# Kernel tuning notes

Hardware: AMD Instinct MI355X
Metric: run time of the kernel (lower is better)

Reference implementation:

```python
import jax, jax.numpy as jnp
import numpy as np

DIM = 256
HEADS = 8
DIM_HEAD = 64
INNER = HEADS * DIM_HEAD  # 512
WIN = 7
N = WIN * WIN  # 49
B = 4096
EPS = 1e-5


def _rel_pos_indices(w):
    pos = np.arange(w)
    gi, gj = np.meshgrid(pos, pos, indexing='ij')
    grid = np.stack([gi.reshape(-1), gj.reshape(-1)], axis=-1)  # (w*w, 2)
    rel = grid[:, None, :] - grid[None, :, :] + (w - 1)          # (n, n, 2)
    return (rel[..., 0] * (2 * w - 1) + rel[..., 1]).astype(np.int32)  # (n, n)


def setup_inputs() -> dict:
    key = jax.random.key(0)
    ks = jax.random.split(key, 6)
    x = jax.random.normal(ks[0], (B, N, DIM), dtype=jnp.float32)
    gamma = jnp.ones((DIM,), dtype=jnp.float32)
    beta = jnp.zeros((DIM,), dtype=jnp.float32)
    W_qkv = jax.random.normal(ks[1], (DIM, 3 * INNER), dtype=jnp.float32) * (DIM ** -0.5)
    W_out = jax.random.normal(ks[2], (INNER, DIM), dtype=jnp.float32) * (INNER ** -0.5)
    b_out = jnp.zeros((DIM,), dtype=jnp.float32)
    bias_table = jax.random.normal(ks[3], ((2 * WIN - 1) ** 2, HEADS), dtype=jnp.float32) * 0.02
    rel_idx = jnp.asarray(_rel_pos_indices(WIN))  # (49, 49) int32
    return {"x": x, "gamma": gamma, "beta": beta, "W_qkv": W_qkv,
            "W_out": W_out, "b_out": b_out, "bias_table": bias_table,
            "rel_idx": rel_idx}


def reference(x, gamma, beta, W_qkv, W_out, b_out, bias_table, rel_idx):
    # LayerNorm
    mu = jnp.mean(x, axis=-1, keepdims=True)
    var = jnp.mean((x - mu) ** 2, axis=-1, keepdims=True)
    xn = (x - mu) * jax.lax.rsqrt(var + EPS) * gamma + beta
    # QKV projection (no bias)
    qkv = xn @ W_qkv                                   # (b, n, 3*inner)
    q, k, v = jnp.split(qkv, 3, axis=-1)
    def to_heads(t):
        b, n, _ = t.shape
        return t.reshape(b, n, HEADS, DIM_HEAD).transpose(0, 2, 1, 3)  # b h n d
    q, k, v = to_heads(q), to_heads(k), to_heads(v)
    q = q * (DIM_HEAD ** -0.5)
    sim = jnp.einsum('bhid,bhjd->bhij', q, k)          # (b, h, n, n)
    bias = bias_table[rel_idx]                         # (n, n, h)
    sim = sim + bias.transpose(2, 0, 1)[None]          # add (h, n, n)
    attn = jax.nn.softmax(sim, axis=-1)
    out = jnp.einsum('bhij,bhjd->bhid', attn, v)       # (b, h, n, d)
    out = out.transpose(0, 2, 1, 3).reshape(x.shape[0], N, INNER)
    return out @ W_out + b_out
```

## Files before the change

kernel.cpp:

```cpp
#include <hip/hip_runtime.h>
#include <hip/hip_bf16.h>
#include <stdint.h>

#define NTOK 49

typedef __bf16 bf16x8 __attribute__((ext_vector_type(8)));
typedef float f32x4 __attribute__((ext_vector_type(4)));

__device__ __forceinline__ uint16_t f2bf(float f){
  uint32_t x = __float_as_uint(f);
  uint32_t r = (x + 0x7fffu + ((x >> 16) & 1u)) >> 16;
  return (uint16_t)r;
}

#define LDS_LD8(buf, row, kelem) \
  __builtin_bit_cast(bf16x8, *(const uint4*)((const char*)(buf) + (row)*128 + ((((kelem)*2)) ^ ((((row))&7)<<4))))

__global__ void prep_kernel(const float* __restrict__ Wqkv,
                            const float* __restrict__ Wout,
                            const float* __restrict__ btab,
                            const int* __restrict__ ridx,
                            uint16_t* __restrict__ WqkvT,
                            uint16_t* __restrict__ WoutT,
                            float* __restrict__ biasPre){
  const int T1 = 1536*256, T2 = 256*512, T3 = 8*2401;
  for (int i = blockIdx.x*blockDim.x + threadIdx.x; i < T1+T2+T3; i += gridDim.x*blockDim.x){
    if (i < T1){ int n = i/256, k = i%256; WqkvT[i] = f2bf(Wqkv[k*1536 + n]); }
    else if (i < T1+T2){ int j = i - T1; int n = j/512, k = j%512; WoutT[j] = f2bf(Wout[k*256 + n]); }
    else { int j = i - T1 - T2; int h = j/2401, ij = j%2401; biasPre[j] = btab[ridx[ij]*8 + h]; }
  }
}

__global__ __launch_bounds__(256, 2)
void maxvit_fused(const float* __restrict__ x,
                  const float* __restrict__ gamma,
                  const float* __restrict__ beta,
                  const uint16_t* __restrict__ WqkvT,
                  const uint16_t* __restrict__ WoutT,
                  const float*    __restrict__ bout,
                  const float*    __restrict__ biasPre,
                  float* __restrict__ out)
{
  __shared__ uint16_t xn[50*256];
  __shared__ uint16_t qs[50*64];
  __shared__ uint16_t ks[50*64];
  __shared__ uint16_t ps[50*64];
  __shared__ uint16_t vt[64*64];

  const int b    = blockIdx.x;
  const int tid  = threadIdx.x;
  const int wave = tid >> 6;
  const int lane = tid & 63;
  const int lo   = lane & 15;
  const int g    = lane >> 4;
  const f32x4 fzero = {0.f, 0.f, 0.f, 0.f};

  {
    const int c0 = lane * 4;
    float4 gm = *(const float4*)(gamma + c0);
    float4 bt = *(const float4*)(beta  + c0);
    for (int r = wave; r < 50; r += 4){
      char* dst = (char*)xn + r*512 + ((c0*2) ^ ((r&7)<<4));
      if (r < NTOK){
        float4 u = *(const float4*)(x + ((size_t)(b*NTOK + r))*256 + c0);
        float s  = u.x+u.y+u.z+u.w;
        float ss = u.x*u.x+u.y*u.y+u.z*u.z+u.w*u.w;
        #pragma unroll
        for (int d = 1; d < 64; d <<= 1){ s += __shfl_xor(s, d); ss += __shfl_xor(ss, d); }
        float mu  = s  * (1.0f/256.0f);
        float var = ss * (1.0f/256.0f) - mu*mu;
        float rs  = rsqrtf(var + 1e-5f);
        ushort4 o;
        o.x = f2bf((u.x-mu)*rs*gm.x+bt.x);
        o.y = f2bf((u.y-mu)*rs*gm.y+bt.y);
        o.z = f2bf((u.z-mu)*rs*gm.z+bt.z);
        o.w = f2bf((u.w-mu)*rs*gm.w+bt.w);
        *(ushort4*)dst = o;
      } else {
        ushort4 z; z.x = z.y = z.z = z.w = 0;
        *(ushort4*)dst = z;
      }
    }
  }
  __syncthreads();

  f32x4 outacc[4][4];
  #pragma unroll
  for (int m = 0; m < 4; m++)
    #pragma unroll
    for (int n = 0; n < 4; n++) outacc[m][n] = fzero;

  for (int h = 0; h < 8; ++h){
    f32x4 aq[4], ak[4], av[4];
    #pragma unroll
    for (int m = 0; m < 4; m++){ aq[m] = fzero; ak[m] = fzero; av[m] = fzero; }
    const uint16_t* pq = WqkvT + (size_t)(       h*64 + wave*16 + lo)*256;
    const uint16_t* pk = WqkvT + (size_t)( 512 + h*64 + wave*16 + lo)*256;
    const uint16_t* pv = WqkvT + (size_t)(1024 + h*64 + wave*16 + lo)*256;
    #pragma unroll
    for (int k0 = 0; k0 < 256; k0 += 32){
      const int kb = k0 + g*8;
      bf16x8 afr[4];
      #pragma unroll
      for (int m = 0; m < 4; m++){
        int row = m*16 + lo;
        if (m == 3) row = (row < 49) ? row : 49;
        afr[m] = __builtin_bit_cast(bf16x8,
          *(const uint4*)((const char*)xn + row*512 + ((kb*2) ^ ((row&7)<<4))));
      }
      bf16x8 fq = __builtin_bit_cast(bf16x8, *(const uint4*)(pq + kb));
      bf16x8 fk = __builtin_bit_cast(bf16x8, *(const uint4*)(pk + kb));
      bf16x8 fv = __builtin_bit_cast(bf16x8, *(const uint4*)(pv + kb));
      #pragma unroll
      for (int m = 0; m < 4; m++){
        aq[m] = __builtin_amdgcn_mfma_f32_16x16x32_bf16(afr[m], fq, aq[m], 0, 0, 0);
        ak[m] = __builtin_amdgcn_mfma_f32_16x16x32_bf16(afr[m], fk, ak[m], 0, 0, 0);
        av[m] = __builtin_amdgcn_mfma_f32_16x16x32_bf16(afr[m], fv, av[m], 0, 0, 0);
      }
    }
    {
      const int d = wave*16 + lo;
      #pragma unroll
      for (int m = 0; m < 4; m++){
        #pragma unroll
        for (int r = 0; r < 4; r++){
          const int token = m*16 + g*4 + r;
          const int tok   = (token < 49) ? token : 49;
          *(uint16_t*)((char*)qs + tok*128 + ((d*2) ^ ((tok&7)<<4))) = f2bf(aq[m][r]*0.125f);
          *(uint16_t*)((char*)ks + tok*128 + ((d*2) ^ ((tok&7)<<4))) = f2bf(ak[m][r]);
          *(uint16_t*)((char*)vt + d*128 + ((token*2) ^ ((d&7)<<4))) = f2bf(av[m][r]);
        }
      }
    }
    __syncthreads();

    f32x4 s[4];
    #pragma unroll
    for (int n = 0; n < 4; n++) s[n] = fzero;
    {
      int qrow = wave*16 + lo; qrow = (qrow < 49) ? qrow : 49;
      bf16x8 a0 = LDS_LD8(qs, qrow, g*8);
      bf16x8 a1 = LDS_LD8(qs, qrow, 32 + g*8);
      #pragma unroll
      for (int n = 0; n < 4; n++){
        int krow = n*16 + lo;
        if (n == 3) krow = (krow < 49) ? krow : 49;
        bf16x8 b0 = LDS_LD8(ks, krow, g*8);
        bf16x8 b1 = LDS_LD8(ks, krow, 32 + g*8);
        s[n] = __builtin_amdgcn_mfma_f32_16x16x32_bf16(a0, b0, s[n], 0, 0, 0);
        s[n] = __builtin_amdgcn_mfma_f32_16x16x32_bf16(a1, b1, s[n], 0, 0, 0);
      }
    }
    {
      const float* bp = biasPre + h*2401;
      #pragma unroll
      for (int n = 0; n < 4; n++){
        const int j = n*16 + lo;
        #pragma unroll
        for (int r = 0; r < 4; r++){
          const int i = wave*16 + g*4 + r;
          float v = s[n][r];
          if (j < NTOK){ if (i < NTOK) v += bp[i*49 + j]; }
          else v = -1e30f;
          s[n][r] = v;
        }
      }
      float mx[4], sm[4];
      #pragma unroll
      for (int r = 0; r < 4; r++){
        float m0 = fmaxf(fmaxf(s[0][r], s[1][r]), fmaxf(s[2][r], s[3][r]));
        #pragma unroll
        for (int d = 1; d < 16; d <<= 1) m0 = fmaxf(m0, __shfl_xor(m0, d));
        mx[r] = m0;
        sm[r] = 0.f;
      }
      #pragma unroll
      for (int n = 0; n < 4; n++)
        #pragma unroll
        for (int r = 0; r < 4; r++){ float p = __expf(s[n][r] - mx[r]); s[n][r] = p; sm[r] += p; }
      #pragma unroll
      for (int r = 0; r < 4; r++){
        float t = sm[r];
        #pragma unroll
        for (int d = 1; d < 16; d <<= 1) t += __shfl_xor(t, d);
        sm[r] = 1.0f / t;
      }
      #pragma unroll
      for (int n = 0; n < 4; n++){
        const int j = n*16 + lo;
        #pragma unroll
        for (int r = 0; r < 4; r++){
          int i = wave*16 + g*4 + r; i = (i < 49) ? i : 49;
          *(uint16_t*)((char*)ps + i*128 + ((j*2) ^ ((i&7)<<4))) = f2bf(s[n][r]*sm[r]);
        }
      }
    }

    f32x4 o[4];
    #pragma unroll
    for (int n = 0; n < 4; n++) o[n] = fzero;
    {
      int prow = wave*16 + lo; prow = (prow < 49) ? prow : 49;
      bf16x8 a0 = LDS_LD8(ps, prow, g*8);
      bf16x8 a1 = LDS_LD8(ps, prow, 32 + g*8);
      #pragma unroll
      for (int n = 0; n < 4; n++){
        const int vrow = n*16 + lo;
        bf16x8 b0 = LDS_LD8(vt, vrow, g*8);
        bf16x8 b1 = LDS_LD8(vt, vrow, 32 + g*8);
        o[n] = __builtin_amdgcn_mfma_f32_16x16x32_bf16(a0, b0, o[n], 0, 0, 0);
        o[n] = __builtin_amdgcn_mfma_f32_16x16x32_bf16(a1, b1, o[n], 0, 0, 0);
      }
    }
    #pragma unroll
    for (int n = 0; n < 4; n++){
      const int d = n*16 + lo;
      #pragma unroll
      for (int r = 0; r < 4; r++){
        int token = wave*16 + g*4 + r; token = (token < 49) ? token : 49;
        *(uint16_t*)((char*)ps + token*128 + ((d*2) ^ ((token&7)<<4))) = f2bf(o[n][r]);
      }
    }
    __syncthreads();

    #pragma unroll
    for (int kk = 0; kk < 2; ++kk){
      const int kb = kk*32 + g*8;
      bf16x8 afr[4];
      #pragma unroll
      for (int m = 0; m < 4; m++){
        int row = m*16 + lo;
        if (m == 3) row = (row < 49) ? row : 49;
        afr[m] = LDS_LD8(ps, row, kb);
      }
      #pragma unroll
      for (int n = 0; n < 4; n++){
        const int ncol = wave*64 + n*16 + lo;
        bf16x8 bb = __builtin_bit_cast(bf16x8,
          *(const uint4*)(WoutT + (size_t)ncol*512 + h*64 + kb));
        #pragma unroll
        for (int m = 0; m < 4; m++)
          outacc[m][n] = __builtin_amdgcn_mfma_f32_16x16x32_bf16(afr[m], bb, outacc[m][n], 0, 0, 0);
      }
    }
  }

  #pragma unroll
  for (int n = 0; n < 4; n++){
    const int col = wave*64 + n*16 + lo;
    const float bo = bout[col];
    #pragma unroll
    for (int m = 0; m < 4; m++){
      #pragma unroll
      for (int r = 0; r < 4; r++){
        const int token = m*16 + g*4 + r;
        if (token < NTOK)
          out[((size_t)(b*NTOK + token))*256 + col] = outacc[m][n][r] + bo;
      }
    }
  }
}

extern "C" void kernel_launch(void* const* d_in, const int* in_sizes, int n_in,
                              void* d_out, int out_size, void* d_ws, size_t ws_size,
                              hipStream_t stream){
  const float* x     = (const float*)d_in[0];
  const float* gamma = (const float*)d_in[1];
  const float* beta  = (const float*)d_in[2];
  const float* Wqkv  = (const float*)d_in[3];
  const float* Wout  = (const float*)d_in[4];
  const float* bout  = (const float*)d_in[5];
  const float* btab  = (const float*)d_in[6];
  const int*   ridx  = (const int*)d_in[7];

  uint16_t* WqkvT   = (uint16_t*)d_ws;
  uint16_t* WoutT   = (uint16_t*)((char*)d_ws + 786432);
  float*    biasPre = (float*)((char*)d_ws + 786432 + 262144);

  prep_kernel<<<512, 256, 0, stream>>>(Wqkv, Wout, btab, ridx, WqkvT, WoutT, biasPre);
  maxvit_fused<<<4096, 256, 0, stream>>>(x, gamma, beta, WqkvT, WoutT, bout, biasPre,
                                         (float*)d_out);
}
```

Measured before the change: 1.083 ms.

## Double-buffer per-head Q/K/V and overlap next-head projection with attention

```diff
diff --git a/kernel.cpp b/kernel.cpp
--- a/kernel.cpp
+++ b/kernel.cpp
@@ -42,10 +42,11 @@
                   float* __restrict__ out)
 {
   __shared__ uint16_t xn[50*256];
-  __shared__ uint16_t qs[50*64];
-  __shared__ uint16_t ks[50*64];
+  __shared__ uint16_t qs[2][50*64];
+  __shared__ uint16_t ks[2][50*64];
+  __shared__ uint16_t vt[2][64*64];
   __shared__ uint16_t ps[50*64];
-  __shared__ uint16_t vt[64*64];
+  __shared__ uint16_t os[50*64];
 
   const int b    = blockIdx.x;
   const int tid  = threadIdx.x;
@@ -90,13 +91,12 @@
     #pragma unroll
     for (int n = 0; n < 4; n++) outacc[m][n] = fzero;
 
-  for (int h = 0; h < 8; ++h){
-    f32x4 aq[4], ak[4], av[4];
-    #pragma unroll
-    for (int m = 0; m < 4; m++){ aq[m] = fzero; ak[m] = fzero; av[m] = fzero; }
-    const uint16_t* pq = WqkvT + (size_t)(       h*64 + wave*16 + lo)*256;
-    const uint16_t* pk = WqkvT + (size_t)( 512 + h*64 + wave*16 + lo)*256;
-    const uint16_t* pv = WqkvT + (size_t)(1024 + h*64 + wave*16 + lo)*256;
+  auto projQK = [&](int hh, int bi){
+    f32x4 aq[4], ak[4];
+    #pragma unroll
+    for (int m = 0; m < 4; m++){ aq[m] = fzero; ak[m] = fzero; }
+    const uint16_t* pq = WqkvT + (size_t)(       hh*64 + wave*16 + lo)*256;
+    const uint16_t* pk = WqkvT + (size_t)( 512 + hh*64 + wave*16 + lo)*256;
     #pragma unroll
     for (int k0 = 0; k0 < 256; k0 += 32){
       const int kb = k0 + g*8;
@@ -110,43 +110,85 @@
       }
       bf16x8 fq = __builtin_bit_cast(bf16x8, *(const uint4*)(pq + kb));
       bf16x8 fk = __builtin_bit_cast(bf16x8, *(const uint4*)(pk + kb));
-      bf16x8 fv = __builtin_bit_cast(bf16x8, *(const uint4*)(pv + kb));
       #pragma unroll
       for (int m = 0; m < 4; m++){
         aq[m] = __builtin_amdgcn_mfma_f32_16x16x32_bf16(afr[m], fq, aq[m], 0, 0, 0);
         ak[m] = __builtin_amdgcn_mfma_f32_16x16x32_bf16(afr[m], fk, ak[m], 0, 0, 0);
+      }
+    }
+    uint16_t* qb = qs[bi];
+    uint16_t* kb2 = ks[bi];
+    const int d = wave*16 + lo;
+    #pragma unroll
+    for (int m = 0; m < 4; m++){
+      #pragma unroll
+      for (int r = 0; r < 4; r++){
+        const int token = m*16 + g*4 + r;
+        const int tok   = (token < 49) ? token : 49;
+        *(uint16_t*)((char*)qb  + tok*128 + ((d*2) ^ ((tok&7)<<4))) = f2bf(aq[m][r]*0.125f);
+        *(uint16_t*)((char*)kb2 + tok*128 + ((d*2) ^ ((tok&7)<<4))) = f2bf(ak[m][r]);
+      }
+    }
+  };
+
+  auto projV = [&](int hh, int bi){
+    f32x4 av[4];
+    #pragma unroll
+    for (int m = 0; m < 4; m++) av[m] = fzero;
+    const uint16_t* pv = WqkvT + (size_t)(1024 + hh*64 + wave*16 + lo)*256;
+    #pragma unroll
+    for (int k0 = 0; k0 < 256; k0 += 32){
+      const int kb = k0 + g*8;
+      bf16x8 afr[4];
+      #pragma unroll
+      for (int m = 0; m < 4; m++){
+        int row = m*16 + lo;
+        if (m == 3) row = (row < 49) ? row : 49;
+        afr[m] = __builtin_bit_cast(bf16x8,
+          *(const uint4*)((const char*)xn + row*512 + ((kb*2) ^ ((row&7)<<4))));
+      }
+      bf16x8 fv = __builtin_bit_cast(bf16x8, *(const uint4*)(pv + kb));
+      #pragma unroll
+      for (int m = 0; m < 4; m++)
         av[m] = __builtin_amdgcn_mfma_f32_16x16x32_bf16(afr[m], fv, av[m], 0, 0, 0);
-      }
-    }
-    {
-      const int d = wave*16 + lo;
-      #pragma unroll
-      for (int m = 0; m < 4; m++){
-        #pragma unroll
-        for (int r = 0; r < 4; r++){
-          const int token = m*16 + g*4 + r;
-          const int tok   = (token < 49) ? token : 49;
-          *(uint16_t*)((char*)qs + tok*128 + ((d*2) ^ ((tok&7)<<4))) = f2bf(aq[m][r]*0.125f);
-          *(uint16_t*)((char*)ks + tok*128 + ((d*2) ^ ((tok&7)<<4))) = f2bf(ak[m][r]);
-          *(uint16_t*)((char*)vt + d*128 + ((token*2) ^ ((d&7)<<4))) = f2bf(av[m][r]);
-        }
-      }
-    }
-    __syncthreads();
+    }
+    uint16_t* vb = vt[bi];
+    const int d = wave*16 + lo;
+    #pragma unroll
+    for (int m = 0; m < 4; m++){
+      #pragma unroll
+      for (int r = 0; r < 4; r++){
+        const int token = m*16 + g*4 + r;
+        *(uint16_t*)((char*)vb + d*128 + ((token*2) ^ ((d&7)<<4))) = f2bf(av[m][r]);
+      }
+    }
+  };
+
+  projQK(0, 0);
+  projV(0, 0);
+  __syncthreads();
+
+  for (int h = 0; h < 8; ++h){
+    const int cur = h & 1, nxt = cur ^ 1;
+    const uint16_t* qsc = qs[cur];
+    const uint16_t* ksc = ks[cur];
+    const uint16_t* vtc = vt[cur];
+
+    if (h < 7) projQK(h+1, nxt);
 
     f32x4 s[4];
     #pragma unroll
     for (int n = 0; n < 4; n++) s[n] = fzero;
     {
       int qrow = wave*16 + lo; qrow = (qrow < 49) ? qrow : 49;
-      bf16x8 a0 = LDS_LD8(qs, qrow, g*8);
-      bf16x8 a1 = LDS_LD8(qs, qrow, 32 + g*8);
+      bf16x8 a0 = LDS_LD8(qsc, qrow, g*8);
+      bf16x8 a1 = LDS_LD8(qsc, qrow, 32 + g*8);
       #pragma unroll
       for (int n = 0; n < 4; n++){
         int krow = n*16 + lo;
         if (n == 3) krow = (krow < 49) ? krow : 49;
-        bf16x8 b0 = LDS_LD8(ks, krow, g*8);
-        bf16x8 b1 = LDS_LD8(ks, krow, 32 + g*8);
+        bf16x8 b0 = LDS_LD8(ksc, krow, g*8);
+        bf16x8 b1 = LDS_LD8(ksc, krow, 32 + g*8);
         s[n] = __builtin_amdgcn_mfma_f32_16x16x32_bf16(a0, b0, s[n], 0, 0, 0);
         s[n] = __builtin_amdgcn_mfma_f32_16x16x32_bf16(a1, b1, s[n], 0, 0, 0);
       }
@@ -206,8 +248,8 @@
       #pragma unroll
       for (int n = 0; n < 4; n++){
         const int vrow = n*16 + lo;
-        bf16x8 b0 = LDS_LD8(vt, vrow, g*8);
-        bf16x8 b1 = LDS_LD8(vt, vrow, 32 + g*8);
+        bf16x8 b0 = LDS_LD8(vtc, vrow, g*8);
+        bf16x8 b1 = LDS_LD8(vtc, vrow, 32 + g*8);
         o[n] = __builtin_amdgcn_mfma_f32_16x16x32_bf16(a0, b0, o[n], 0, 0, 0);
         o[n] = __builtin_amdgcn_mfma_f32_16x16x32_bf16(a1, b1, o[n], 0, 0, 0);
       }
@@ -218,10 +260,12 @@
       #pragma unroll
       for (int r = 0; r < 4; r++){
         int token = wave*16 + g*4 + r; token = (token < 49) ? token : 49;
-        *(uint16_t*)((char*)ps + token*128 + ((d*2) ^ ((token&7)<<4))) = f2bf(o[n][r]);
+        *(uint16_t*)((char*)os + token*128 + ((d*2) ^ ((token&7)<<4))) = f2bf(o[n][r]);
       }
     }
     __syncthreads();
+
+    if (h < 7) projV(h+1, nxt);
 
     #pragma unroll
     for (int kk = 0; kk < 2; ++kk){
@@ -231,7 +275,7 @@
       for (int m = 0; m < 4; m++){
         int row = m*16 + lo;
         if (m == 3) row = (row < 49) ? row : 49;
-        afr[m] = LDS_LD8(ps, row, kb);
+        afr[m] = LDS_LD8(os, row, kb);
       }
       #pragma unroll
       for (int n = 0; n < 4; n++){
@@ -243,6 +287,7 @@
           outacc[m][n] = __builtin_amdgcn_mfma_f32_16x16x32_bf16(afr[m], bb, outacc[m][n], 0, 0, 0);
       }
     }
+    __syncthreads();
   }
 
   #pragma unroll
```

Measured after the change: 870.5 us. 19.6% less time.

## Split fused MaxViT attention across eight waves per block

Applied to the files above, without the earlier changes.

```diff
diff --git a/kernel.cpp b/kernel.cpp
--- a/kernel.cpp
+++ b/kernel.cpp
@@ -31,7 +31,7 @@
   }
 }
 
-__global__ __launch_bounds__(256, 2)
+__global__ __launch_bounds__(512, 4)
 void maxvit_fused(const float* __restrict__ x,
                   const float* __restrict__ gamma,
                   const float* __restrict__ beta,
@@ -44,8 +44,9 @@
   __shared__ uint16_t xn[50*256];
   __shared__ uint16_t qs[50*64];
   __shared__ uint16_t ks[50*64];
+  __shared__ uint16_t vt[64*64];
   __shared__ uint16_t ps[50*64];
-  __shared__ uint16_t vt[64*64];
+  __shared__ uint16_t os[50*64];
 
   const int b    = blockIdx.x;
   const int tid  = threadIdx.x;
@@ -53,13 +54,15 @@
   const int lane = tid & 63;
   const int lo   = lane & 15;
   const int g    = lane >> 4;
+  const int wm   = wave & 3;
+  const int wn   = wave >> 2;
   const f32x4 fzero = {0.f, 0.f, 0.f, 0.f};
 
   {
     const int c0 = lane * 4;
     float4 gm = *(const float4*)(gamma + c0);
     float4 bt = *(const float4*)(beta  + c0);
-    for (int r = wave; r < 50; r += 4){
+    for (int r = wave; r < 50; r += 8){
       char* dst = (char*)xn + r*512 + ((c0*2) ^ ((r&7)<<4));
       if (r < NTOK){
         float4 u = *(const float4*)(x + ((size_t)(b*NTOK + r))*256 + c0);
@@ -84,61 +87,65 @@
   }
   __syncthreads();
 
-  f32x4 outacc[4][4];
+  f32x4 outacc[4][2];
   #pragma unroll
-  for (int m = 0; m < 4; m++)
-    #pragma unroll
-    for (int n = 0; n < 4; n++) outacc[m][n] = fzero;
+  for (int m = 0; m < 4; m++){ outacc[m][0] = fzero; outacc[m][1] = fzero; }
+
+  const int mt     = wave >> 1;
+  const int ntbase = (wave & 1) * 6;
 
   for (int h = 0; h < 8; ++h){
-    f32x4 aq[4], ak[4], av[4];
-    #pragma unroll
-    for (int m = 0; m < 4; m++){ aq[m] = fzero; ak[m] = fzero; av[m] = fzero; }
-    const uint16_t* pq = WqkvT + (size_t)(       h*64 + wave*16 + lo)*256;
-    const uint16_t* pk = WqkvT + (size_t)( 512 + h*64 + wave*16 + lo)*256;
-    const uint16_t* pv = WqkvT + (size_t)(1024 + h*64 + wave*16 + lo)*256;
-    #pragma unroll
-    for (int k0 = 0; k0 < 256; k0 += 32){
-      const int kb = k0 + g*8;
-      bf16x8 afr[4];
-      #pragma unroll
-      for (int m = 0; m < 4; m++){
-        int row = m*16 + lo;
-        if (m == 3) row = (row < 49) ? row : 49;
-        afr[m] = __builtin_bit_cast(bf16x8,
-          *(const uint4*)((const char*)xn + row*512 + ((kb*2) ^ ((row&7)<<4))));
-      }
-      bf16x8 fq = __builtin_bit_cast(bf16x8, *(const uint4*)(pq + kb));
-      bf16x8 fk = __builtin_bit_cast(bf16x8, *(const uint4*)(pk + kb));
-      bf16x8 fv = __builtin_bit_cast(bf16x8, *(const uint4*)(pv + kb));
-      #pragma unroll
-      for (int m = 0; m < 4; m++){
-        aq[m] = __builtin_amdgcn_mfma_f32_16x16x32_bf16(afr[m], fq, aq[m], 0, 0, 0);
-        ak[m] = __builtin_amdgcn_mfma_f32_16x16x32_bf16(afr[m], fk, ak[m], 0, 0, 0);
-        av[m] = __builtin_amdgcn_mfma_f32_16x16x32_bf16(afr[m], fv, av[m], 0, 0, 0);
-      }
-    }
     {
-      const int d = wave*16 + lo;
-      #pragma unroll
-      for (int m = 0; m < 4; m++){
+      f32x4 acc[6];
+      #pragma unroll
+      for (int t = 0; t < 6; t++) acc[t] = fzero;
+      const uint16_t* wp[6];
+      #pragma unroll
+      for (int t = 0; t < 6; t++){
+        const int nt  = ntbase + t;
+        const int sel = nt >> 2;
+        const int dt  = nt & 3;
+        wp[t] = WqkvT + (size_t)(sel*512 + h*64 + dt*16 + lo)*256;
+      }
+      int xrow = mt*16 + lo;
+      if (mt == 3) xrow = (xrow < 49) ? xrow : 49;
+      #pragma unroll
+      for (int k0 = 0; k0 < 256; k0 += 32){
+        const int kb = k0 + g*8;
+        bf16x8 afr = __builtin_bit_cast(bf16x8,
+          *(const uint4*)((const char*)xn + xrow*512 + ((kb*2) ^ ((xrow&7)<<4))));
+        #pragma unroll
+        for (int t = 0; t < 6; t++){
+          bf16x8 bb = __builtin_bit_cast(bf16x8, *(const uint4*)(wp[t] + kb));
+          acc[t] = __builtin_amdgcn_mfma_f32_16x16x32_bf16(afr, bb, acc[t], 0, 0, 0);
+        }
+      }
+      #pragma unroll
+      for (int t = 0; t < 6; t++){
+        const int nt  = ntbase + t;
+        const int sel = nt >> 2;
+        const int d   = (nt & 3)*16 + lo;
         #pragma unroll
         for (int r = 0; r < 4; r++){
-          const int token = m*16 + g*4 + r;
-          const int tok   = (token < 49) ? token : 49;
-          *(uint16_t*)((char*)qs + tok*128 + ((d*2) ^ ((tok&7)<<4))) = f2bf(aq[m][r]*0.125f);
-          *(uint16_t*)((char*)ks + tok*128 + ((d*2) ^ ((tok&7)<<4))) = f2bf(ak[m][r]);
-          *(uint16_t*)((char*)vt + d*128 + ((token*2) ^ ((d&7)<<4))) = f2bf(av[m][r]);
+          const int token = mt*16 + g*4 + r;
+          if (sel == 2){
+            *(uint16_t*)((char*)vt + d*128 + ((token*2) ^ ((d&7)<<4))) = f2bf(acc[t][r]);
+          } else {
+            const int tok = (token < 49) ? token : 49;
+            uint16_t* buf = (sel == 0) ? qs : ks;
+            const float v = (sel == 0) ? acc[t][r]*0.125f : acc[t][r];
+            *(uint16_t*)((char*)buf + tok*128 + ((d*2) ^ ((tok&7)<<4))) = f2bf(v);
+          }
         }
       }
     }
     __syncthreads();
 
-    f32x4 s[4];
-    #pragma unroll
-    for (int n = 0; n < 4; n++) s[n] = fzero;
     {
-      int qrow = wave*16 + lo; qrow = (qrow < 49) ? qrow : 49;
+      f32x4 s[4];
+      #pragma unroll
+      for (int n = 0; n < 4; n++) s[n] = fzero;
+      int qrow = wm*16 + lo; qrow = (qrow < 49) ? qrow : 49;
       bf16x8 a0 = LDS_LD8(qs, qrow, g*8);
       bf16x8 a1 = LDS_LD8(qs, qrow, 32 + g*8);
       #pragma unroll
@@ -150,15 +157,13 @@
         s[n] = __builtin_amdgcn_mfma_f32_16x16x32_bf16(a0, b0, s[n], 0, 0, 0);
         s[n] = __builtin_amdgcn_mfma_f32_16x16x32_bf16(a1, b1, s[n], 0, 0, 0);
       }
-    }
-    {
       const float* bp = biasPre + h*2401;
       #pragma unroll
       for (int n = 0; n < 4; n++){
         const int j = n*16 + lo;
         #pragma unroll
         for (int r = 0; r < 4; r++){
-          const int i = wave*16 + g*4 + r;
+          const int i = wm*16 + g*4 + r;
           float v = s[n][r];
           if (j < NTOK){ if (i < NTOK) v += bp[i*49 + j]; }
           else v = -1e30f;
@@ -185,40 +190,42 @@
         for (int d = 1; d < 16; d <<= 1) t += __shfl_xor(t, d);
         sm[r] = 1.0f / t;
       }
-      #pragma unroll
-      for (int n = 0; n < 4; n++){
-        const int j = n*16 + lo;
-        #pragma unroll
-        for (int r = 0; r < 4; r++){
-          int i = wave*16 + g*4 + r; i = (i < 49) ? i : 49;
-          *(uint16_t*)((char*)ps + i*128 + ((j*2) ^ ((i&7)<<4))) = f2bf(s[n][r]*sm[r]);
-        }
-      }
-    }
-
-    f32x4 o[4];
-    #pragma unroll
-    for (int n = 0; n < 4; n++) o[n] = fzero;
+      if (wn == 0){
+        #pragma unroll
+        for (int n = 0; n < 4; n++){
+          const int j = n*16 + lo;
+          #pragma unroll
+          for (int r = 0; r < 4; r++){
+            int i = wm*16 + g*4 + r; i = (i < 49) ? i : 49;
+            *(uint16_t*)((char*)ps + i*128 + ((j*2) ^ ((i&7)<<4))) = f2bf(s[n][r]*sm[r]);
+          }
+        }
+      }
+    }
+    __syncthreads();
+
     {
-      int prow = wave*16 + lo; prow = (prow < 49) ? prow : 49;
+      f32x4 o[2];
+      o[0] = fzero; o[1] = fzero;
+      int prow = wm*16 + lo; prow = (prow < 49) ? prow : 49;
       bf16x8 a0 = LDS_LD8(ps, prow, g*8);
       bf16x8 a1 = LDS_LD8(ps, prow, 32 + g*8);
       #pragma unroll
-      for (int n = 0; n < 4; n++){
-        const int vrow = n*16 + lo;
+      for (int n2 = 0; n2 < 2; n2++){
+        const int vrow = wn*32 + n2*16 + lo;
         bf16x8 b0 = LDS_LD8(vt, vrow, g*8);
         bf16x8 b1 = LDS_LD8(vt, vrow, 32 + g*8);
-        o[n] = __builtin_amdgcn_mfma_f32_16x16x32_bf16(a0, b0, o[n], 0, 0, 0);
-        o[n] = __builtin_amdgcn_mfma_f32_16x16x32_bf16(a1, b1, o[n], 0, 0, 0);
-      }
-    }
-    #pragma unroll
-    for (int n = 0; n < 4; n++){
-      const int d = n*16 + lo;
-      #pragma unroll
-      for (int r = 0; r < 4; r++){
-        int token = wave*16 + g*4 + r; token = (token < 49) ? token : 49;
-        *(uint16_t*)((char*)ps + token*128 + ((d*2) ^ ((token&7)<<4))) = f2bf(o[n][r]);
+        o[n2] = __builtin_amdgcn_mfma_f32_16x16x32_bf16(a0, b0, o[n2], 0, 0, 0);
+        o[n2] = __builtin_amdgcn_mfma_f32_16x16x32_bf16(a1, b1, o[n2], 0, 0, 0);
+      }
+      #pragma unroll
+      for (int n2 = 0; n2 < 2; n2++){
+        const int d = wn*32 + n2*16 + lo;
+        #pragma unroll
+        for (int r = 0; r < 4; r++){
+          int token = wm*16 + g*4 + r; token = (token < 49) ? token : 49;
+          *(uint16_t*)((char*)os + token*128 + ((d*2) ^ ((token&7)<<4))) = f2bf(o[n2][r]);
+        }
       }
     }
     __syncthreads();
@@ -231,31 +238,33 @@
       for (int m = 0; m < 4; m++){
         int row = m*16 + lo;
         if (m == 3) row = (row < 49) ? row : 49;
-        afr[m] = LDS_LD8(ps, row, kb);
-      }
-      #pragma unroll
-      for (int n = 0; n < 4; n++){
-        const int ncol = wave*64 + n*16 + lo;
+        afr[m] = LDS_LD8(os, row, kb);
+      }
+      #pragma unroll
+      for (int n2 = 0; n2 < 2; n2++){
+        const int ncol = wave*32 + n2*16 + lo;
         bf16x8 bb = __builtin_bit_cast(bf16x8,
           *(const uint4*)(WoutT + (size_t)ncol*512 + h*64 + kb));
         #pragma unroll
         for (int m = 0; m < 4; m++)
-          outacc[m][n] = __builtin_amdgcn_mfma_f32_16x16x32_bf16(afr[m], bb, outacc[m][n], 0, 0, 0);
-      }
-    }
-  }
-
-  #pragma unroll
-  for (int n = 0; n < 4; n++){
-    const int col = wave*64 + n*16 + lo;
-    const float bo = bout[col];
+          outacc[m][n2] = __builtin_amdgcn_mfma_f32_16x16x32_bf16(afr[m], bb, outacc[m][n2], 0, 0, 0);
+      }
+    }
+  }
+
+  {
+    float bo0 = bout[wave*32 + lo];
+    float bo1 = bout[wave*32 + 16 + lo];
     #pragma unroll
     for (int m = 0; m < 4; m++){
       #pragma unroll
       for (int r = 0; r < 4; r++){
         const int token = m*16 + g*4 + r;
-        if (token < NTOK)
-          out[((size_t)(b*NTOK + token))*256 + col] = outacc[m][n][r] + bo;
+        if (token < NTOK){
+          float* po = out + ((size_t)(b*NTOK + token))*256 + wave*32 + lo;
+          po[0]  = outacc[m][0][r] + bo0;
+          po[16] = outacc[m][1][r] + bo1;
+        }
       }
     }
   }
@@ -278,6 +287,6 @@
   float*    biasPre = (float*)((char*)d_ws + 786432 + 262144);
 
   prep_kernel<<<512, 256, 0, stream>>>(Wqkv, Wout, btab, ridx, WqkvT, WoutT, biasPre);
-  maxvit_fused<<<4096, 256, 0, stream>>>(x, gamma, beta, WqkvT, WoutT, bout, biasPre,
+  maxvit_fused<<<4096, 512, 0, stream>>>(x, gamma, beta, WqkvT, WoutT, bout, biasPre,
                                          (float*)d_out);
 }
```

Result: slower. 2.783 ms (+156.9%).

## Split fused attention kernel into QKV-attention and separate output-projection kernels

Applied to the files above, without the earlier changes.

```diff
diff --git a/kernel.cpp b/kernel.cpp
--- a/kernel.cpp
+++ b/kernel.cpp
@@ -15,6 +15,10 @@
 
 #define LDS_LD8(buf, row, kelem) \
   __builtin_bit_cast(bf16x8, *(const uint4*)((const char*)(buf) + (row)*128 + ((((kelem)*2)) ^ ((((row))&7)<<4))))
+#define LDS_LD8X(buf, row, kelem) \
+  __builtin_bit_cast(bf16x8, *(const uint4*)((const char*)(buf) + (row)*512 + ((((kelem)*2)) ^ ((((row))&7)<<4))))
+#define LDS_LD8O(buf, row, kelem) \
+  __builtin_bit_cast(bf16x8, *(const uint4*)((const char*)(buf) + (row)*1024 + ((((kelem)*2)) ^ ((((row))&7)<<4))))
 
 __global__ void prep_kernel(const float* __restrict__ Wqkv,
                             const float* __restrict__ Wout,
@@ -31,15 +35,13 @@
   }
 }
 
-__global__ __launch_bounds__(256, 2)
-void maxvit_fused(const float* __restrict__ x,
-                  const float* __restrict__ gamma,
-                  const float* __restrict__ beta,
-                  const uint16_t* __restrict__ WqkvT,
-                  const uint16_t* __restrict__ WoutT,
-                  const float*    __restrict__ bout,
-                  const float*    __restrict__ biasPre,
-                  float* __restrict__ out)
+__global__ __launch_bounds__(256, 3)
+void qkv_attn(const float* __restrict__ x,
+              const float* __restrict__ gamma,
+              const float* __restrict__ beta,
+              const uint16_t* __restrict__ WqkvT,
+              const float*    __restrict__ biasPre,
+              uint16_t* __restrict__ Ostg)
 {
   __shared__ uint16_t xn[50*256];
   __shared__ uint16_t qs[50*64];
@@ -84,41 +86,34 @@
   }
   __syncthreads();
 
-  f32x4 outacc[4][4];
-  #pragma unroll
-  for (int m = 0; m < 4; m++)
-    #pragma unroll
-    for (int n = 0; n < 4; n++) outacc[m][n] = fzero;
-
   for (int h = 0; h < 8; ++h){
-    f32x4 aq[4], ak[4], av[4];
-    #pragma unroll
-    for (int m = 0; m < 4; m++){ aq[m] = fzero; ak[m] = fzero; av[m] = fzero; }
-    const uint16_t* pq = WqkvT + (size_t)(       h*64 + wave*16 + lo)*256;
-    const uint16_t* pk = WqkvT + (size_t)( 512 + h*64 + wave*16 + lo)*256;
-    const uint16_t* pv = WqkvT + (size_t)(1024 + h*64 + wave*16 + lo)*256;
-    #pragma unroll
-    for (int k0 = 0; k0 < 256; k0 += 32){
-      const int kb = k0 + g*8;
-      bf16x8 afr[4];
-      #pragma unroll
-      for (int m = 0; m < 4; m++){
-        int row = m*16 + lo;
-        if (m == 3) row = (row < 49) ? row : 49;
-        afr[m] = __builtin_bit_cast(bf16x8,
-          *(const uint4*)((const char*)xn + row*512 + ((kb*2) ^ ((row&7)<<4))));
-      }
-      bf16x8 fq = __builtin_bit_cast(bf16x8, *(const uint4*)(pq + kb));
-      bf16x8 fk = __builtin_bit_cast(bf16x8, *(const uint4*)(pk + kb));
-      bf16x8 fv = __builtin_bit_cast(bf16x8, *(const uint4*)(pv + kb));
-      #pragma unroll
-      for (int m = 0; m < 4; m++){
-        aq[m] = __builtin_amdgcn_mfma_f32_16x16x32_bf16(afr[m], fq, aq[m], 0, 0, 0);
-        ak[m] = __builtin_amdgcn_mfma_f32_16x16x32_bf16(afr[m], fk, ak[m], 0, 0, 0);
-        av[m] = __builtin_amdgcn_mfma_f32_16x16x32_bf16(afr[m], fv, av[m], 0, 0, 0);
-      }
-    }
-    {
+    {
+      f32x4 aq[4], ak[4], av[4];
+      #pragma unroll
+      for (int m = 0; m < 4; m++){ aq[m] = fzero; ak[m] = fzero; av[m] = fzero; }
+      const uint16_t* pq = WqkvT + (size_t)(       h*64 + wave*16 + lo)*256;
+      const uint16_t* pk = WqkvT + (size_t)( 512 + h*64 + wave*16 + lo)*256;
+      const uint16_t* pv = WqkvT + (size_t)(1024 + h*64 + wave*16 + lo)*256;
+      #pragma unroll
+      for (int k0 = 0; k0 < 256; k0 += 32){
+        const int kb = k0 + g*8;
+        bf16x8 afr[4];
+        #pragma unroll
+        for (int m = 0; m < 4; m++){
+          int row = m*16 + lo;
+          if (m == 3) row = (row < 49) ? row : 49;
+          afr[m] = LDS_LD8X(xn, row, kb);
+        }
+        bf16x8 fq = __builtin_bit_cast(bf16x8, *(const uint4*)(pq + kb));
+        bf16x8 fk = __builtin_bit_cast(bf16x8, *(const uint4*)(pk + kb));
+        bf16x8 fv = __builtin_bit_cast(bf16x8, *(const uint4*)(pv + kb));
+        #pragma unroll
+        for (int m = 0; m < 4; m++){
+          aq[m] = __builtin_amdgcn_mfma_f32_16x16x32_bf16(afr[m], fq, aq[m], 0, 0, 0);
+          ak[m] = __builtin_amdgcn_mfma_f32_16x16x32_bf16(afr[m], fk, ak[m], 0, 0, 0);
+          av[m] = __builtin_amdgcn_mfma_f32_16x16x32_bf16(afr[m], fv, av[m], 0, 0, 0);
+        }
+      }
       const int d = wave*16 + lo;
       #pragma unroll
       for (int m = 0; m < 4; m++){
@@ -212,36 +207,76 @@
         o[n] = __builtin_amdgcn_mfma_f32_16x16x32_bf16(a1, b1, o[n], 0, 0, 0);
       }
     }
+    {
+      uint16_t* owin = Ostg + (size_t)b*(NTOK*512);
+      #pragma unroll
+      for (int n = 0; n < 4; n++){
+        const int d = n*16 + lo;
+        #pragma unroll
+        for (int r = 0; r < 4; r++){
+          const int token = wave*16 + g*4 + r;
+          if (token < NTOK)
+            owin[token*512 + h*64 + d] = f2bf(o[n][r]);
+        }
+      }
+    }
+    __syncthreads();
+  }
+}
+
+__global__ __launch_bounds__(256, 2)
+void outproj(const uint16_t* __restrict__ Ostg,
+             const uint16_t* __restrict__ WoutT,
+             const float*    __restrict__ bout,
+             float* __restrict__ out)
+{
+  __shared__ uint16_t os[50*512];
+
+  const int b    = blockIdx.x;
+  const int tid  = threadIdx.x;
+  const int wave = tid >> 6;
+  const int lane = tid & 63;
+  const int lo   = lane & 15;
+  const int g    = lane >> 4;
+  const f32x4 fzero = {0.f, 0.f, 0.f, 0.f};
+
+  {
+    const uint16_t* src = Ostg + (size_t)b*(NTOK*512);
+    for (int idx = tid; idx < 50*64; idx += 256){
+      const int row = idx >> 6;
+      const int c   = idx & 63;
+      uint4 v;
+      if (row < NTOK) v = *(const uint4*)(src + (size_t)row*512 + c*8);
+      else { v.x = v.y = v.z = v.w = 0u; }
+      *(uint4*)((char*)os + row*1024 + ((c*16) ^ ((row&7)<<4))) = v;
+    }
+  }
+  __syncthreads();
+
+  f32x4 outacc[4][4];
+  #pragma unroll
+  for (int m = 0; m < 4; m++)
+    #pragma unroll
+    for (int n = 0; n < 4; n++) outacc[m][n] = fzero;
+
+  #pragma unroll
+  for (int k0 = 0; k0 < 512; k0 += 32){
+    const int kb = k0 + g*8;
+    bf16x8 afr[4];
+    #pragma unroll
+    for (int m = 0; m < 4; m++){
+      int row = m*16 + lo;
+      if (m == 3) row = (row < 49) ? row : 49;
+      afr[m] = LDS_LD8O(os, row, kb);
+    }
     #pragma unroll
     for (int n = 0; n < 4; n++){
-      const int d = n*16 + lo;
-      #pragma unroll
-      for (int r = 0; r < 4; r++){
-        int token = wave*16 + g*4 + r; token = (token < 49) ? token : 49;
-        *(uint16_t*)((char*)ps + token*128 + ((d*2) ^ ((token&7)<<4))) = f2bf(o[n][r]);
-      }
-    }
-    __syncthreads();
-
-    #pragma unroll
-    for (int kk = 0; kk < 2; ++kk){
-      const int kb = kk*32 + g*8;
-      bf16x8 afr[4];
-      #pragma unroll
-      for (int m = 0; m < 4; m++){
-        int row = m*16 + lo;
-        if (m == 3) row = (row < 49) ? row : 49;
-        afr[m] = LDS_LD8(ps, row, kb);
-      }
-      #pragma unroll
-      for (int n = 0; n < 4; n++){
-        const int ncol = wave*64 + n*16 + lo;
-        bf16x8 bb = __builtin_bit_cast(bf16x8,
-          *(const uint4*)(WoutT + (size_t)ncol*512 + h*64 + kb));
-        #pragma unroll
-        for (int m = 0; m < 4; m++)
-          outacc[m][n] = __builtin_amdgcn_mfma_f32_16x16x32_bf16(afr[m], bb, outacc[m][n], 0, 0, 0);
-      }
+      const int ncol = wave*64 + n*16 + lo;
+      bf16x8 bb = __builtin_bit_cast(bf16x8,
+        *(const uint4*)(WoutT + (size_t)ncol*512 + kb));
+      #pragma unroll
+      for (int m = 0; m < 4; m++)
+        outacc[m][n] = __builtin_amdgcn_mfma_f32_16x16x32_bf16(afr[m], bb, outacc[m][n], 0, 0, 0);
     }
   }
 
@@ -255,7 +290,7 @@
       for (int r = 0; r < 4; r++){
         const int token = m*16 + g*4 + r;
         if (token < NTOK)
-          out[((size_t)(b*NTOK + token))*256 + col] = outacc[m][n][r] + bo;
+          out[((size_t)b*NTOK + token)*256 + col] = outacc[m][n][r] + bo;
       }
     }
   }
@@ -277,7 +312,9 @@
   uint16_t* WoutT   = (uint16_t*)((char*)d_ws + 786432);
   float*    biasPre = (float*)((char*)d_ws + 786432 + 262144);
 
+  uint16_t* Ostg = (uint16_t*)d_out;
+
   prep_kernel<<<512, 256, 0, stream>>>(Wqkv, Wout, btab, ridx, WqkvT, WoutT, biasPre);
-  maxvit_fused<<<4096, 256, 0, stream>>>(x, gamma, beta, WqkvT, WoutT, bout, biasPre,
-                                         (float*)d_out);
-}
+  qkv_attn<<<4096, 256, 0, stream>>>(x, gamma, beta, WqkvT, biasPre, Ostg);
+  outproj<<<4096, 256, 0, stream>>>(Ostg, WoutT, bout, (float*)d_out);
+}
```

Result: slower. 1.290 ms (+19.2%).
